# Kernel optimization log

Hardware: AMD Instinct MI355X
Metric: run time of the kernel (lower is better)

The kernel has to match this reference:

```python
import jax, jax.numpy as jnp
import numpy as np

NUM_USERS = 100000
NUM_ITEMS = 50000
EMB_DIM = 64
USER_FEAT = 256
ITEM_FEAT = 256
NUM_EDGES = 1000000
NUM_LAYERS = 4
N = NUM_USERS + NUM_ITEMS


def setup_inputs() -> dict:
    key = jax.random.key(0)
    ks = jax.random.split(key, 8)
    edge_index = jax.random.randint(ks[0], (2, NUM_EDGES), 0, N, dtype=jnp.int64 if jax.config.x64_enabled else jnp.int32).astype(jnp.int32)
    emb_users = jax.random.normal(ks[1], (NUM_USERS, EMB_DIM), dtype=jnp.float32) * 0.1
    emb_items = jax.random.normal(ks[2], (NUM_ITEMS, EMB_DIM), dtype=jnp.float32) * 0.1
    users_features = jax.random.normal(ks[3], (NUM_USERS, USER_FEAT), dtype=jnp.float32)
    items_features = jax.random.normal(ks[4], (NUM_ITEMS, ITEM_FEAT), dtype=jnp.float32)
    # original init is zeros; use small random weights for a non-trivial baseline
    user_proj_w = jax.random.normal(ks[5], (EMB_DIM, USER_FEAT), dtype=jnp.float32) * 0.01
    item_proj_w = jax.random.normal(ks[6], (EMB_DIM, ITEM_FEAT), dtype=jnp.float32) * 0.01
    return {
        "edge_index": edge_index,
        "emb_users": emb_users,
        "emb_items": emb_items,
        "users_features": users_features,
        "items_features": items_features,
        "user_proj_w": user_proj_w,
        "item_proj_w": item_proj_w,
    }


def reference(edge_index, emb_users, emb_items, users_features, items_features, user_proj_w, item_proj_w):
    row, col = edge_index[0], edge_index[1]
    # symmetric GCN normalization without self-loops (PyG LGConv)
    deg = jax.ops.segment_sum(jnp.ones_like(col, dtype=emb_users.dtype), col, num_segments=N)
    dinv = jnp.where(deg > 0, jax.lax.rsqrt(jnp.maximum(deg, 1.0)), 0.0)
    norm = dinv[row] * dinv[col]  # [E]

    x = jnp.concatenate([emb_users, emb_items], axis=0)  # [N, D]
    acc = x
    for _ in range(NUM_LAYERS):
        msgs = x[row] * norm[:, None]                      # [E, D] gather + scale
        x = jax.ops.segment_sum(msgs, col, num_segments=N)  # scatter-add
        acc = acc + x
    # mean over (L+1) layer embeddings, then extra 1/(L+1) factor (faithful to source)
    emb_final = acc / ((NUM_LAYERS + 1) ** 2)

    u_final = emb_final[:NUM_USERS] + users_features @ user_proj_w.T
    i_final = emb_final[NUM_USERS:] + items_features @ item_proj_w.T
    return (u_final, i_final)
```

## Files before the change

kernel.cpp:

```cpp
#include <hip/hip_runtime.h>

#define U_NODES 100000
#define I_NODES 50000
#define N_NODES 150000
#define EMB_D   64
#define FEAT_K  256
#define N_LAYERS 4

typedef __attribute__((ext_vector_type(8))) short short8;
typedef __attribute__((ext_vector_type(4))) float f32x4;

static __device__ __forceinline__ unsigned short f2bf(float f) {
    unsigned u = __builtin_bit_cast(unsigned, f);
    u += 0x7fffu + ((u >> 16) & 1u);
    return (unsigned short)(u >> 16);
}
static __device__ __forceinline__ float bflo(unsigned u) {
    return __builtin_bit_cast(float, u << 16);
}
static __device__ __forceinline__ float bfhi(unsigned u) {
    return __builtin_bit_cast(float, u & 0xffff0000u);
}

__global__ __launch_bounds__(256) void k_count(const int* __restrict__ col,
                                               int* __restrict__ deg, int E) {
    int e = blockIdx.x * 256 + threadIdx.x;
    if (e < E) atomicAdd(&deg[col[e]], 1);
}

__global__ __launch_bounds__(256) void k_dinv(const int* __restrict__ deg,
                                              float* __restrict__ dinv, int n) {
    int i = blockIdx.x * 256 + threadIdx.x;
    if (i < n) {
        int d = deg[i];
        dinv[i] = (d > 0) ? rsqrtf((float)d) : 0.0f;
    }
}

__global__ __launch_bounds__(256) void k_scan_a(const int* __restrict__ deg,
                                                int* __restrict__ rs,
                                                int* __restrict__ bsum, int n) {
    __shared__ int wsum[4];
    int t = threadIdx.x;
    int i = blockIdx.x * 256 + t;
    int v = (i < n) ? deg[i] : 0;
    int x = v;
    #pragma unroll
    for (int off = 1; off < 64; off <<= 1) {
        int y = __shfl_up(x, off, 64);
        if ((t & 63) >= off) x += y;
    }
    if ((t & 63) == 63) wsum[t >> 6] = x;
    __syncthreads();
    int base = 0;
    #pragma unroll
    for (int w = 0; w < 4; ++w) base += (w < (t >> 6)) ? wsum[w] : 0;
    if (i < n) rs[i] = base + x - v;
    if (t == 255) bsum[blockIdx.x] = base + x;
}

__global__ __launch_bounds__(1024) void k_scan_b(int* __restrict__ bs, int nb) {
    __shared__ int wsum[16];
    int t = threadIdx.x;
    int v = (t < nb) ? bs[t] : 0;
    int x = v;
    #pragma unroll
    for (int off = 1; off < 64; off <<= 1) {
        int y = __shfl_up(x, off, 64);
        if ((t & 63) >= off) x += y;
    }
    if ((t & 63) == 63) wsum[t >> 6] = x;
    __syncthreads();
    int base = 0;
    #pragma unroll
    for (int w = 0; w < 16; ++w) base += (w < (t >> 6)) ? wsum[w] : 0;
    if (t < nb) bs[t] = base + x - v;
}

__global__ __launch_bounds__(256) void k_scan_c(int* __restrict__ rs,
                                                const int* __restrict__ bsum,
                                                int* __restrict__ cursor,
                                                int n, int E) {
    int i = blockIdx.x * 256 + threadIdx.x;
    if (i < n) {
        int v = rs[i] + bsum[blockIdx.x];
        rs[i] = v;
        cursor[i] = v;
    }
    if (i == 0) rs[n] = E;
}

__global__ __launch_bounds__(256) void k_fill(const int* __restrict__ row,
                                              const int* __restrict__ col,
                                              const float* __restrict__ dinv,
                                              int* __restrict__ cursor,
                                              int2* __restrict__ csr, int E) {
    int e = blockIdx.x * 256 + threadIdx.x;
    if (e < E) {
        int r = row[e], c = col[e];
        int p = atomicAdd(&cursor[c], 1);
        int2 v;
        v.x = r;
        v.y = __builtin_bit_cast(int, dinv[r] * dinv[c]);
        csr[p] = v;
    }
}

__global__ __launch_bounds__(256) void k_cvtw(const float* __restrict__ wu,
                                              const float* __restrict__ wi,
                                              unsigned short* __restrict__ wub,
                                              unsigned short* __restrict__ wib) {
    int i = blockIdx.x * 256 + threadIdx.x;
    if (i < EMB_D * FEAT_K) wub[i] = f2bf(wu[i]);
    else                    wib[i - EMB_D * FEAT_K] = f2bf(wi[i - EMB_D * FEAT_K]);
}

__global__ __launch_bounds__(256) void k_init(const float4* __restrict__ eu,
                                              const float4* __restrict__ ei,
                                              uint4* __restrict__ x,
                                              int n8u, int n8) {
    int i = blockIdx.x * 256 + threadIdx.x;
    if (i >= n8) return;
    const float4* s = (i < n8u) ? (eu + (size_t)i * 2) : (ei + (size_t)(i - n8u) * 2);
    float4 p0 = s[0], p1 = s[1];
    uint4 r;
    r.x = (unsigned)f2bf(p0.x) | ((unsigned)f2bf(p0.y) << 16);
    r.y = (unsigned)f2bf(p0.z) | ((unsigned)f2bf(p0.w) << 16);
    r.z = (unsigned)f2bf(p1.x) | ((unsigned)f2bf(p1.y) << 16);
    r.w = (unsigned)f2bf(p1.z) | ((unsigned)f2bf(p1.w) << 16);
    x[i] = r;
}

#define ACC8(v_, w_)                       \
    s0 = fmaf(bflo((v_).x), (w_), s0);     \
    s1 = fmaf(bfhi((v_).x), (w_), s1);     \
    s2 = fmaf(bflo((v_).y), (w_), s2);     \
    s3 = fmaf(bfhi((v_).y), (w_), s3);     \
    s4 = fmaf(bflo((v_).z), (w_), s4);     \
    s5 = fmaf(bfhi((v_).z), (w_), s5);     \
    s6 = fmaf(bflo((v_).w), (w_), s6);     \
    s7 = fmaf(bfhi((v_).w), (w_), s7);

#define GATHER4(xsrc_, ep_, em_)                                              \
    {                                                                         \
        int i0_ = (ep_), i1_ = min((ep_) + 1, (em_));                         \
        int i2_ = min((ep_) + 2, (em_)), i3_ = min((ep_) + 3, (em_));         \
        int2 pa_ = csr[i0_], pb_ = csr[i1_], pc_ = csr[i2_], pd_ = csr[i3_];  \
        float wa_ = __builtin_bit_cast(float, pa_.y);                         \
        float wb_ = ((ep_) + 1 <= (em_)) ? __builtin_bit_cast(float, pb_.y) : 0.f; \
        float wc_ = ((ep_) + 2 <= (em_)) ? __builtin_bit_cast(float, pc_.y) : 0.f; \
        float wd_ = ((ep_) + 3 <= (em_)) ? __builtin_bit_cast(float, pd_.y) : 0.f; \
        uint4 va_ = (xsrc_)[(size_t)pa_.x * 8 + lane];                        \
        uint4 vb_ = (xsrc_)[(size_t)pb_.x * 8 + lane];                        \
        uint4 vc_ = (xsrc_)[(size_t)pc_.x * 8 + lane];                        \
        uint4 vd_ = (xsrc_)[(size_t)pd_.x * 8 + lane];                        \
        ACC8(va_, wa_) ACC8(vb_, wb_) ACC8(vc_, wc_) ACC8(vd_, wd_)           \
    }

__global__ __launch_bounds__(256) void k_agg(const uint4* __restrict__ xin,
                                             uint4* __restrict__ xout,
                                             const int* __restrict__ rs,
                                             const int2* __restrict__ csr,
                                             int n_nodes) {
    int idx = blockIdx.x * 256 + threadIdx.x;
    int node = idx >> 3;
    int lane = idx & 7;
    if (node >= n_nodes) return;
    int e0 = rs[node], e1 = rs[node + 1];
    float s0 = 0.f, s1 = 0.f, s2 = 0.f, s3 = 0.f;
    float s4 = 0.f, s5 = 0.f, s6 = 0.f, s7 = 0.f;
    int em = e1 - 1;
    for (int ep = e0; ep < e1; ep += 4) GATHER4(xin, ep, em)
    uint4 r;
    r.x = (unsigned)f2bf(s0) | ((unsigned)f2bf(s1) << 16);
    r.y = (unsigned)f2bf(s2) | ((unsigned)f2bf(s3) << 16);
    r.z = (unsigned)f2bf(s4) | ((unsigned)f2bf(s5) << 16);
    r.w = (unsigned)f2bf(s6) | ((unsigned)f2bf(s7) << 16);
    xout[(size_t)node * 8 + lane] = r;
}

__global__ __launch_bounds__(256) void k_agg4(const uint4* __restrict__ x3,
                                              const uint4* __restrict__ x1,
                                              const uint4* __restrict__ x2,
                                              const float* __restrict__ embU,
                                              const float* __restrict__ embI,
                                              float* __restrict__ outp,
                                              const int* __restrict__ rs,
                                              const int2* __restrict__ csr,
                                              int n_nodes, int U) {
    int idx = blockIdx.x * 256 + threadIdx.x;
    int node = idx >> 3;
    int lane = idx & 7;
    if (node >= n_nodes) return;
    int e0 = rs[node], e1 = rs[node + 1];
    float s0 = 0.f, s1 = 0.f, s2 = 0.f, s3 = 0.f;
    float s4 = 0.f, s5 = 0.f, s6 = 0.f, s7 = 0.f;
    int em = e1 - 1;
    for (int ep = e0; ep < e1; ep += 4) GATHER4(x3, ep, em)
    uint4 v1 = x1[(size_t)node * 8 + lane];
    uint4 v2 = x2[(size_t)node * 8 + lane];
    uint4 v3 = x3[(size_t)node * 8 + lane];
    const float* ebp = (node < U) ? (embU + (size_t)node * EMB_D)
                                  : (embI + (size_t)(node - U) * EMB_D);
    float4 ea = ((const float4*)ebp)[lane * 2];
    float4 eb2 = ((const float4*)ebp)[lane * 2 + 1];
    const float sc = 1.0f / 25.0f;
    float4 o0, o1;
    o0.x = (ea.x  + bflo(v1.x) + bflo(v2.x) + bflo(v3.x) + s0) * sc;
    o0.y = (ea.y  + bfhi(v1.x) + bfhi(v2.x) + bfhi(v3.x) + s1) * sc;
    o0.z = (ea.z  + bflo(v1.y) + bflo(v2.y) + bflo(v3.y) + s2) * sc;
    o0.w = (ea.w  + bfhi(v1.y) + bfhi(v2.y) + bfhi(v3.y) + s3) * sc;
    o1.x = (eb2.x + bflo(v1.z) + bflo(v2.z) + bflo(v3.z) + s4) * sc;
    o1.y = (eb2.y + bfhi(v1.z) + bfhi(v2.z) + bfhi(v3.z) + s5) * sc;
    o1.z = (eb2.z + bflo(v1.w) + bflo(v2.w) + bflo(v3.w) + s6) * sc;
    o1.w = (eb2.w + bfhi(v1.w) + bfhi(v2.w) + bfhi(v3.w) + s7) * sc;
    float4* op = (float4*)(outp + (size_t)node * EMB_D) + lane * 2;
    op[0] = o0;
    op[1] = o1;
}

__global__ __launch_bounds__(256) void k_projm(const float* __restrict__ FU,
                                               const float* __restrict__ FI,
                                               const unsigned short* __restrict__ WUb,
                                               const unsigned short* __restrict__ WIb,
                                               float* __restrict__ out,
                                               int nbU, int U, int I) {
    __shared__ uint4 sB[2048];
    const bool isU = ((int)blockIdx.x < nbU);
    const uint4* __restrict__ Wb4 = (const uint4*)(isU ? WUb : WIb);
    #pragma unroll
    for (int i = 0; i < 8; ++i) {
        int d = threadIdx.x + i * 256;
        int kk = d >> 6, nt = (d >> 4) & 3, c = d & 15;
        sB[d] = Wb4[(size_t)(nt * 16 + c) * 32 + kk];
    }

    const float* __restrict__ F = isU ? FU : FI;
    float* __restrict__ o = isU ? out : out + (size_t)U * EMB_D;
    const int M = isU ? U : I;
    const int wave = threadIdx.x >> 6;
    const int lane = threadIdx.x & 63;
    const int l15  = lane & 15;
    const int kq   = lane >> 4;
    const int row0 = (isU ? (int)blockIdx.x : (int)blockIdx.x - nbU) * 64 + wave * 16;
    const int arow = min(row0 + l15, M - 1);
    const float* fb = F + (size_t)arow * FEAT_K + kq * 8;

    float4 a0 = ((const float4*)(fb +   0))[0], a1 = ((const float4*)(fb +   0))[1];
    float4 a2 = ((const float4*)(fb +  32))[0], a3 = ((const float4*)(fb +  32))[1];
    float4 a4 = ((const float4*)(fb +  64))[0], a5 = ((const float4*)(fb +  64))[1];
    float4 a6 = ((const float4*)(fb +  96))[0], a7 = ((const float4*)(fb +  96))[1];
    float4 a8 = ((const float4*)(fb + 128))[0], a9 = ((const float4*)(fb + 128))[1];
    float4 aa = ((const float4*)(fb + 160))[0], ab = ((const float4*)(fb + 160))[1];
    float4 ac = ((const float4*)(fb + 192))[0], ad = ((const float4*)(fb + 192))[1];
    float4 ae = ((const float4*)(fb + 224))[0], af = ((const float4*)(fb + 224))[1];

    __syncthreads();

    f32x4 acc0 = {0.f, 0.f, 0.f, 0.f};
    f32x4 acc1 = {0.f, 0.f, 0.f, 0.f};
    f32x4 acc2 = {0.f, 0.f, 0.f, 0.f};
    f32x4 acc3 = {0.f, 0.f, 0.f, 0.f};

#define CVT2(d_, lo_, hi_) asm("v_cvt_pk_bf16_f32 %0, %1, %2" : "=v"(d_) : "v"(lo_), "v"(hi_))
#define KSTEP(ks_, xa_, ya_)                                                   \
    {                                                                          \
        unsigned p0, p1, p2, p3;                                               \
        CVT2(p0, (xa_).x, (xa_).y); CVT2(p1, (xa_).z, (xa_).w);                \
        CVT2(p2, (ya_).x, (ya_).y); CVT2(p3, (ya_).z, (ya_).w);                \
        uint4 up; up.x = p0; up.y = p1; up.z = p2; up.w = p3;                  \
        short8 av = __builtin_bit_cast(short8, up);                            \
        const uint4* sbk = &sB[((ks_) * 4 + kq) * 64];                         \
        short8 b0 = __builtin_bit_cast(short8, sbk[l15]);                      \
        short8 b1 = __builtin_bit_cast(short8, sbk[16 + l15]);                 \
        short8 b2 = __builtin_bit_cast(short8, sbk[32 + l15]);                 \
        short8 b3 = __builtin_bit_cast(short8, sbk[48 + l15]);                 \
        acc0 = __builtin_amdgcn_mfma_f32_16x16x32_bf16(av, b0, acc0, 0, 0, 0); \
        acc1 = __builtin_amdgcn_mfma_f32_16x16x32_bf16(av, b1, acc1, 0, 0, 0); \
        acc2 = __builtin_amdgcn_mfma_f32_16x16x32_bf16(av, b2, acc2, 0, 0, 0); \
        acc3 = __builtin_amdgcn_mfma_f32_16x16x32_bf16(av, b3, acc3, 0, 0, 0); \
    }

    KSTEP(0, a0, a1) KSTEP(1, a2, a3) KSTEP(2, a4, a5) KSTEP(3, a6, a7)
    KSTEP(4, a8, a9) KSTEP(5, aa, ab) KSTEP(6, ac, ad) KSTEP(7, ae, af)
#undef KSTEP
#undef CVT2

    #pragma unroll
    for (int r = 0; r < 4; ++r) {
        int grow = row0 + kq * 4 + r;
        if (grow < M) {
            float* op = o + (size_t)grow * EMB_D + l15;
            op[0]  += acc0[r];
            op[16] += acc1[r];
            op[32] += acc2[r];
            op[48] += acc3[r];
        }
    }
}

extern "C" void kernel_launch(void* const* d_in, const int* in_sizes, int n_in,
                              void* d_out, int out_size, void* d_ws, size_t ws_size,
                              hipStream_t stream) {
    const int E = in_sizes[0] / 2;
    const int N = N_NODES, U = U_NODES;

    const int*   edge  = (const int*)d_in[0];
    const float* emb_u = (const float*)d_in[1];
    const float* emb_i = (const float*)d_in[2];
    const float* fu    = (const float*)d_in[3];
    const float* fi    = (const float*)d_in[4];
    const float* wu    = (const float*)d_in[5];
    const float* wi    = (const float*)d_in[6];
    const int* row = edge;
    const int* col = edge + E;

    char* p = (char*)d_ws;
    auto carve = [&](size_t bytes) -> void* {
        void* q = (void*)p;
        p += (bytes + 255) & ~(size_t)255;
        return q;
    };
    float* dinv    = (float*)carve((size_t)N * 4);
    int*   deg     = (int*)  carve((size_t)N * 4);
    int*   rs      = (int*)  carve((size_t)(N + 1) * 4);
    int*   cursor  = (int*)  carve((size_t)N * 4);
    int*   bsum    = (int*)  carve(1024 * 4);
    int2*  csr     = (int2*) carve((size_t)E * 8);
    unsigned short* wub = (unsigned short*)carve((size_t)EMB_D * FEAT_K * 2);
    unsigned short* wib = (unsigned short*)carve((size_t)EMB_D * FEAT_K * 2);
    uint4* x0 = (uint4*)carve((size_t)N * EMB_D * 2);
    uint4* x1 = (uint4*)carve((size_t)N * EMB_D * 2);
    uint4* x2 = (uint4*)carve((size_t)N * EMB_D * 2);
    uint4* x3 = (uint4*)carve((size_t)N * EMB_D * 2);

    float* outp = (float*)d_out;

    const int NB  = (N + 255) / 256;
    const int EB  = (E + 255) / 256;
    const int XB8 = ((N * 8) + 255) / 256;

    hipMemsetAsync(deg, 0, (size_t)N * 4, stream);
    k_count<<<EB, 256, 0, stream>>>(col, deg, E);
    k_dinv<<<NB, 256, 0, stream>>>(deg, dinv, N);
    k_scan_a<<<NB, 256, 0, stream>>>(deg, rs, bsum, N);
    k_scan_b<<<1, 1024, 0, stream>>>(bsum, NB);
    k_scan_c<<<NB, 256, 0, stream>>>(rs, bsum, cursor, N, E);
    k_fill<<<EB, 256, 0, stream>>>(row, col, dinv, cursor, csr, E);
    k_cvtw<<<(2 * EMB_D * FEAT_K) / 256, 256, 0, stream>>>(wu, wi, wub, wib);
    k_init<<<XB8, 256, 0, stream>>>((const float4*)emb_u, (const float4*)emb_i,
                                    x0, U * 8, N * 8);
    k_agg<<<XB8, 256, 0, stream>>>(x0, x1, rs, csr, N);
    k_agg<<<XB8, 256, 0, stream>>>(x1, x2, rs, csr, N);
    k_agg<<<XB8, 256, 0, stream>>>(x2, x3, rs, csr, N);
    k_agg4<<<XB8, 256, 0, stream>>>(x3, x1, x2, emb_u, emb_i, outp, rs, csr, N, U);
    const int nbU = (U + 63) / 64;
    const int nbI = (N - U + 63) / 64;
    k_projm<<<nbU + nbI, 256, 0, stream>>>(fu, fi, wub, wib, outp, nbU, U, N - U);
}
```

Before: 275.5 us.

## Store only source index in CSR and compute edge norm from dinv on the fly

The CSR entries shrink from (src, norm) int2 pairs to plain int source indices, written with nontemporal stores. Each aggregation layer now rebuilds the edge weight as dinv[src]*dinv[node]. This halves CSR traffic per layer and removes the dinv gathers from the fill kernel. The cost is an extra random dinv gather per edge in every layer, and an empty asm barrier is added in the projection kernel to pin load scheduling.

```diff
diff --git a/kernel.cpp b/kernel.cpp
--- a/kernel.cpp
+++ b/kernel.cpp
@@ -92,17 +92,13 @@
 
 __global__ __launch_bounds__(256) void k_fill(const int* __restrict__ row,
                                               const int* __restrict__ col,
-                                              const float* __restrict__ dinv,
                                               int* __restrict__ cursor,
-                                              int2* __restrict__ csr, int E) {
+                                              int* __restrict__ csr_src, int E) {
     int e = blockIdx.x * 256 + threadIdx.x;
     if (e < E) {
         int r = row[e], c = col[e];
         int p = atomicAdd(&cursor[c], 1);
-        int2 v;
-        v.x = r;
-        v.y = __builtin_bit_cast(int, dinv[r] * dinv[c]);
-        csr[p] = v;
+        __builtin_nontemporal_store(r, &csr_src[p]);
     }
 }
 
@@ -141,36 +137,39 @@
     s6 = fmaf(bflo((v_).w), (w_), s6);     \
     s7 = fmaf(bfhi((v_).w), (w_), s7);
 
-#define GATHER4(xsrc_, ep_, em_)                                              \
+#define GATHER4(xsrc_, ep_, em_, dn_)                                         \
     {                                                                         \
         int i0_ = (ep_), i1_ = min((ep_) + 1, (em_));                         \
         int i2_ = min((ep_) + 2, (em_)), i3_ = min((ep_) + 3, (em_));         \
-        int2 pa_ = csr[i0_], pb_ = csr[i1_], pc_ = csr[i2_], pd_ = csr[i3_];  \
-        float wa_ = __builtin_bit_cast(float, pa_.y);                         \
-        float wb_ = ((ep_) + 1 <= (em_)) ? __builtin_bit_cast(float, pb_.y) : 0.f; \
-        float wc_ = ((ep_) + 2 <= (em_)) ? __builtin_bit_cast(float, pc_.y) : 0.f; \
-        float wd_ = ((ep_) + 3 <= (em_)) ? __builtin_bit_cast(float, pd_.y) : 0.f; \
-        uint4 va_ = (xsrc_)[(size_t)pa_.x * 8 + lane];                        \
-        uint4 vb_ = (xsrc_)[(size_t)pb_.x * 8 + lane];                        \
-        uint4 vc_ = (xsrc_)[(size_t)pc_.x * 8 + lane];                        \
-        uint4 vd_ = (xsrc_)[(size_t)pd_.x * 8 + lane];                        \
+        int sa_ = csr_src[i0_], sb_ = csr_src[i1_];                           \
+        int sc_ = csr_src[i2_], sd_ = csr_src[i3_];                           \
+        float wa_ = dinv[sa_] * (dn_);                                        \
+        float wb_ = ((ep_) + 1 <= (em_)) ? dinv[sb_] * (dn_) : 0.f;           \
+        float wc_ = ((ep_) + 2 <= (em_)) ? dinv[sc_] * (dn_) : 0.f;           \
+        float wd_ = ((ep_) + 3 <= (em_)) ? dinv[sd_] * (dn_) : 0.f;           \
+        uint4 va_ = (xsrc_)[(size_t)sa_ * 8 + lane];                          \
+        uint4 vb_ = (xsrc_)[(size_t)sb_ * 8 + lane];                          \
+        uint4 vc_ = (xsrc_)[(size_t)sc_ * 8 + lane];                          \
+        uint4 vd_ = (xsrc_)[(size_t)sd_ * 8 + lane];                          \
         ACC8(va_, wa_) ACC8(vb_, wb_) ACC8(vc_, wc_) ACC8(vd_, wd_)           \
     }
 
 __global__ __launch_bounds__(256) void k_agg(const uint4* __restrict__ xin,
                                              uint4* __restrict__ xout,
                                              const int* __restrict__ rs,
-                                             const int2* __restrict__ csr,
+                                             const int* __restrict__ csr_src,
+                                             const float* __restrict__ dinv,
                                              int n_nodes) {
     int idx = blockIdx.x * 256 + threadIdx.x;
     int node = idx >> 3;
     int lane = idx & 7;
     if (node >= n_nodes) return;
     int e0 = rs[node], e1 = rs[node + 1];
+    float dn = dinv[node];
     float s0 = 0.f, s1 = 0.f, s2 = 0.f, s3 = 0.f;
     float s4 = 0.f, s5 = 0.f, s6 = 0.f, s7 = 0.f;
     int em = e1 - 1;
-    for (int ep = e0; ep < e1; ep += 4) GATHER4(xin, ep, em)
+    for (int ep = e0; ep < e1; ep += 4) GATHER4(xin, ep, em, dn)
     uint4 r;
     r.x = (unsigned)f2bf(s0) | ((unsigned)f2bf(s1) << 16);
     r.y = (unsigned)f2bf(s2) | ((unsigned)f2bf(s3) << 16);
@@ -186,17 +185,19 @@
                                               const float* __restrict__ embI,
                                               float* __restrict__ outp,
                                               const int* __restrict__ rs,
-                                              const int2* __restrict__ csr,
+                                              const int* __restrict__ csr_src,
+                                              const float* __restrict__ dinv,
                                               int n_nodes, int U) {
     int idx = blockIdx.x * 256 + threadIdx.x;
     int node = idx >> 3;
     int lane = idx & 7;
     if (node >= n_nodes) return;
     int e0 = rs[node], e1 = rs[node + 1];
+    float dn = dinv[node];
     float s0 = 0.f, s1 = 0.f, s2 = 0.f, s3 = 0.f;
     float s4 = 0.f, s5 = 0.f, s6 = 0.f, s7 = 0.f;
     int em = e1 - 1;
-    for (int ep = e0; ep < e1; ep += 4) GATHER4(x3, ep, em)
+    for (int ep = e0; ep < e1; ep += 4) GATHER4(x3, ep, em, dn)
     uint4 v1 = x1[(size_t)node * 8 + lane];
     uint4 v2 = x2[(size_t)node * 8 + lane];
     uint4 v3 = x3[(size_t)node * 8 + lane];
@@ -254,6 +255,11 @@
     float4 aa = ((const float4*)(fb + 160))[0], ab = ((const float4*)(fb + 160))[1];
     float4 ac = ((const float4*)(fb + 192))[0], ad = ((const float4*)(fb + 192))[1];
     float4 ae = ((const float4*)(fb + 224))[0], af = ((const float4*)(fb + 224))[1];
+    asm volatile(""
+        : "+v"(a0.x), "+v"(a1.x), "+v"(a2.x), "+v"(a3.x),
+          "+v"(a4.x), "+v"(a5.x), "+v"(a6.x), "+v"(a7.x),
+          "+v"(a8.x), "+v"(a9.x), "+v"(aa.x), "+v"(ab.x),
+          "+v"(ac.x), "+v"(ad.x), "+v"(ae.x), "+v"(af.x));
 
     __syncthreads();
 
@@ -315,6 +321,10 @@
     const int* row = edge;
     const int* col = edge + E;
 
+    const int NB  = (N + 255) / 256;
+    const int EB  = (E + 255) / 256;
+    const int XB8 = ((N * 8) + 255) / 256;
+
     char* p = (char*)d_ws;
     auto carve = [&](size_t bytes) -> void* {
         void* q = (void*)p;
@@ -326,7 +336,7 @@
     int*   rs      = (int*)  carve((size_t)(N + 1) * 4);
     int*   cursor  = (int*)  carve((size_t)N * 4);
     int*   bsum    = (int*)  carve(1024 * 4);
-    int2*  csr     = (int2*) carve((size_t)E * 8);
+    int*   csr_src = (int*)  carve((size_t)E * 4);
     unsigned short* wub = (unsigned short*)carve((size_t)EMB_D * FEAT_K * 2);
     unsigned short* wib = (unsigned short*)carve((size_t)EMB_D * FEAT_K * 2);
     uint4* x0 = (uint4*)carve((size_t)N * EMB_D * 2);
@@ -336,24 +346,20 @@
 
     float* outp = (float*)d_out;
 
-    const int NB  = (N + 255) / 256;
-    const int EB  = (E + 255) / 256;
-    const int XB8 = ((N * 8) + 255) / 256;
-
     hipMemsetAsync(deg, 0, (size_t)N * 4, stream);
     k_count<<<EB, 256, 0, stream>>>(col, deg, E);
     k_dinv<<<NB, 256, 0, stream>>>(deg, dinv, N);
     k_scan_a<<<NB, 256, 0, stream>>>(deg, rs, bsum, N);
     k_scan_b<<<1, 1024, 0, stream>>>(bsum, NB);
     k_scan_c<<<NB, 256, 0, stream>>>(rs, bsum, cursor, N, E);
-    k_fill<<<EB, 256, 0, stream>>>(row, col, dinv, cursor, csr, E);
+    k_fill<<<EB, 256, 0, stream>>>(row, col, cursor, csr_src, E);
     k_cvtw<<<(2 * EMB_D * FEAT_K) / 256, 256, 0, stream>>>(wu, wi, wub, wib);
     k_init<<<XB8, 256, 0, stream>>>((const float4*)emb_u, (const float4*)emb_i,
                                     x0, U * 8, N * 8);
-    k_agg<<<XB8, 256, 0, stream>>>(x0, x1, rs, csr, N);
-    k_agg<<<XB8, 256, 0, stream>>>(x1, x2, rs, csr, N);
-    k_agg<<<XB8, 256, 0, stream>>>(x2, x3, rs, csr, N);
-    k_agg4<<<XB8, 256, 0, stream>>>(x3, x1, x2, emb_u, emb_i, outp, rs, csr, N, U);
+    k_agg<<<XB8, 256, 0, stream>>>(x0, x1, rs, csr_src, dinv, N);
+    k_agg<<<XB8, 256, 0, stream>>>(x1, x2, rs, csr_src, dinv, N);
+    k_agg<<<XB8, 256, 0, stream>>>(x2, x3, rs, csr_src, dinv, N);
+    k_agg4<<<XB8, 256, 0, stream>>>(x3, x1, x2, emb_u, emb_i, outp, rs, csr_src, dinv, N, U);
     const int nbU = (U + 63) / 64;
     const int nbI = (N - U + 63) / 64;
     k_projm<<<nbU + nbI, 256, 0, stream>>>(fu, fi, wub, wib, outp, nbU, U, N - U);
```

Result: slower. 317.0 us (+15.0%).

## Restructure projection GEMM: 16-row tiles via LDS, weights held in registers

Applied to the files above, without the earlier changes.

The projection kernel now handles 16 rows per block instead of 64. Each wave owns a 16-column slice of the output and keeps its bf16 weight fragments in registers, where before the whole weight matrix was staged in LDS. The feature rows are loaded straight into swizzled LDS with global_load_lds, and every wave reads the same A tile, converts it to bf16 and issues 8 MFMAs. This removes the per-block LDS copy of the weights and raises block count, at the cost of four times as many blocks that each re-read the 32 KB weight matrix (likely served from cache).

```diff
diff --git a/kernel.cpp b/kernel.cpp
--- a/kernel.cpp
+++ b/kernel.cpp
@@ -225,76 +225,66 @@
                                                const unsigned short* __restrict__ WIb,
                                                float* __restrict__ out,
                                                int nbU, int U, int I) {
-    __shared__ uint4 sB[2048];
+    __shared__ float sA[16 * 256];
     const bool isU = ((int)blockIdx.x < nbU);
+    const float* __restrict__ F = isU ? FU : FI;
     const uint4* __restrict__ Wb4 = (const uint4*)(isU ? WUb : WIb);
-    #pragma unroll
-    for (int i = 0; i < 8; ++i) {
-        int d = threadIdx.x + i * 256;
-        int kk = d >> 6, nt = (d >> 4) & 3, c = d & 15;
-        sB[d] = Wb4[(size_t)(nt * 16 + c) * 32 + kk];
-    }
-
-    const float* __restrict__ F = isU ? FU : FI;
     float* __restrict__ o = isU ? out : out + (size_t)U * EMB_D;
     const int M = isU ? U : I;
+    const int tile = isU ? (int)blockIdx.x : (int)blockIdx.x - nbU;
+    const int row0 = tile * 16;
     const int wave = threadIdx.x >> 6;
     const int lane = threadIdx.x & 63;
     const int l15  = lane & 15;
     const int kq   = lane >> 4;
-    const int row0 = (isU ? (int)blockIdx.x : (int)blockIdx.x - nbU) * 64 + wave * 16;
-    const int arow = min(row0 + l15, M - 1);
-    const float* fb = F + (size_t)arow * FEAT_K + kq * 8;
-
-    float4 a0 = ((const float4*)(fb +   0))[0], a1 = ((const float4*)(fb +   0))[1];
-    float4 a2 = ((const float4*)(fb +  32))[0], a3 = ((const float4*)(fb +  32))[1];
-    float4 a4 = ((const float4*)(fb +  64))[0], a5 = ((const float4*)(fb +  64))[1];
-    float4 a6 = ((const float4*)(fb +  96))[0], a7 = ((const float4*)(fb +  96))[1];
-    float4 a8 = ((const float4*)(fb + 128))[0], a9 = ((const float4*)(fb + 128))[1];
-    float4 aa = ((const float4*)(fb + 160))[0], ab = ((const float4*)(fb + 160))[1];
-    float4 ac = ((const float4*)(fb + 192))[0], ad = ((const float4*)(fb + 192))[1];
-    float4 ae = ((const float4*)(fb + 224))[0], af = ((const float4*)(fb + 224))[1];
-
+
+    const uint4* wp = Wb4 + (size_t)(wave * 16 + l15) * 32 + kq;
+    uint4 B0 = wp[0],  B1 = wp[4],  B2 = wp[8],  B3 = wp[12];
+    uint4 B4 = wp[16], B5 = wp[20], B6 = wp[24], B7 = wp[28];
+
+    #pragma unroll
+    for (int j = 0; j < 4; ++j) {
+        int r = wave * 4 + j;
+        int grow = min(row0 + r, M - 1);
+        int sboff = (lane * 16) ^ ((r & 7) << 4);
+        const float* src = F + (size_t)grow * FEAT_K + (sboff >> 2);
+        __builtin_amdgcn_global_load_lds(
+            (const __attribute__((address_space(1))) void*)src,
+            (__attribute__((address_space(3))) void*)(sA + r * 256),
+            16, 0, 0);
+    }
     __syncthreads();
 
-    f32x4 acc0 = {0.f, 0.f, 0.f, 0.f};
-    f32x4 acc1 = {0.f, 0.f, 0.f, 0.f};
-    f32x4 acc2 = {0.f, 0.f, 0.f, 0.f};
-    f32x4 acc3 = {0.f, 0.f, 0.f, 0.f};
+    f32x4 acc = {0.f, 0.f, 0.f, 0.f};
+    const char* arow_p = (const char*)(sA + l15 * 256);
+    const int sw = (l15 & 7) << 4;
 
 #define CVT2(d_, lo_, hi_) asm("v_cvt_pk_bf16_f32 %0, %1, %2" : "=v"(d_) : "v"(lo_), "v"(hi_))
-#define KSTEP(ks_, xa_, ya_)                                                   \
+#define KS(ks_, B_)                                                            \
     {                                                                          \
+        int cb = (ks_) * 128 + kq * 32;                                        \
+        f32x4 lo = *(const f32x4*)(arow_p + ((cb) ^ sw));                      \
+        f32x4 hi = *(const f32x4*)(arow_p + ((cb + 16) ^ sw));                 \
         unsigned p0, p1, p2, p3;                                               \
-        CVT2(p0, (xa_).x, (xa_).y); CVT2(p1, (xa_).z, (xa_).w);                \
-        CVT2(p2, (ya_).x, (ya_).y); CVT2(p3, (ya_).z, (ya_).w);                \
+        CVT2(p0, lo[0], lo[1]); CVT2(p1, lo[2], lo[3]);                        \
+        CVT2(p2, hi[0], hi[1]); CVT2(p3, hi[2], hi[3]);                        \
         uint4 up; up.x = p0; up.y = p1; up.z = p2; up.w = p3;                  \
         short8 av = __builtin_bit_cast(short8, up);                            \
-        const uint4* sbk = &sB[((ks_) * 4 + kq) * 64];                         \
-        short8 b0 = __builtin_bit_cast(short8, sbk[l15]);                      \
-        short8 b1 = __builtin_bit_cast(short8, sbk[16 + l15]);                 \
-        short8 b2 = __builtin_bit_cast(short8, sbk[32 + l15]);                 \
-        short8 b3 = __builtin_bit_cast(short8, sbk[48 + l15]);                 \
-        acc0 = __builtin_amdgcn_mfma_f32_16x16x32_bf16(av, b0, acc0, 0, 0, 0); \
-        acc1 = __builtin_amdgcn_mfma_f32_16x16x32_bf16(av, b1, acc1, 0, 0, 0); \
-        acc2 = __builtin_amdgcn_mfma_f32_16x16x32_bf16(av, b2, acc2, 0, 0, 0); \
-        acc3 = __builtin_amdgcn_mfma_f32_16x16x32_bf16(av, b3, acc3, 0, 0, 0); \
-    }
-
-    KSTEP(0, a0, a1) KSTEP(1, a2, a3) KSTEP(2, a4, a5) KSTEP(3, a6, a7)
-    KSTEP(4, a8, a9) KSTEP(5, aa, ab) KSTEP(6, ac, ad) KSTEP(7, ae, af)
-#undef KSTEP
+        short8 bv = __builtin_bit_cast(short8, B_);                            \
+        acc = __builtin_amdgcn_mfma_f32_16x16x32_bf16(av, bv, acc, 0, 0, 0);   \
+    }
+
+    KS(0, B0) KS(1, B1) KS(2, B2) KS(3, B3)
+    KS(4, B4) KS(5, B5) KS(6, B6) KS(7, B7)
+#undef KS
 #undef CVT2
 
     #pragma unroll
     for (int r = 0; r < 4; ++r) {
         int grow = row0 + kq * 4 + r;
         if (grow < M) {
-            float* op = o + (size_t)grow * EMB_D + l15;
-            op[0]  += acc0[r];
-            op[16] += acc1[r];
-            op[32] += acc2[r];
-            op[48] += acc3[r];
+            float* op = o + (size_t)grow * EMB_D + wave * 16 + l15;
+            op[0] += acc[r];
         }
     }
 }
@@ -314,6 +304,10 @@
     const float* wi    = (const float*)d_in[6];
     const int* row = edge;
     const int* col = edge + E;
+
+    const int NB  = (N + 255) / 256;
+    const int EB  = (E + 255) / 256;
+    const int XB8 = ((N * 8) + 255) / 256;
 
     char* p = (char*)d_ws;
     auto carve = [&](size_t bytes) -> void* {
@@ -336,10 +330,6 @@
 
     float* outp = (float*)d_out;
 
-    const int NB  = (N + 255) / 256;
-    const int EB  = (E + 255) / 256;
-    const int XB8 = ((N * 8) + 255) / 256;
-
     hipMemsetAsync(deg, 0, (size_t)N * 4, stream);
     k_count<<<EB, 256, 0, stream>>>(col, deg, E);
     k_dinv<<<NB, 256, 0, stream>>>(deg, dinv, N);
@@ -354,7 +344,7 @@
     k_agg<<<XB8, 256, 0, stream>>>(x1, x2, rs, csr, N);
     k_agg<<<XB8, 256, 0, stream>>>(x2, x3, rs, csr, N);
     k_agg4<<<XB8, 256, 0, stream>>>(x3, x1, x2, emb_u, emb_i, outp, rs, csr, N, U);
-    const int nbU = (U + 63) / 64;
-    const int nbI = (N - U + 63) / 64;
+    const int nbU = (U + 15) / 16;
+    const int nbI = (N - U + 15) / 16;
     k_projm<<<nbU + nbI, 256, 0, stream>>>(fu, fi, wub, wib, outp, nbU, U, N - U);
 }
```

New measurement: 280.8 us. Within noise of the previous version (+1.9%).
